# Kernel tuning notes

Hardware: AMD Instinct MI355X
Metric: run time of the kernel (lower is better)

The kernel has to match this reference:

```python
import jax, jax.numpy as jnp
import numpy as np

N = 100_000      # nodes
E = 1_600_000    # edges (avg degree 16)
D_IN = 64
D_HID = 64
D_OUT = 16


def setup_inputs() -> dict:
    key = jax.random.key(0)
    ks = jax.random.split(key, 12)
    x = jax.random.normal(ks[0], (N, D_IN), jnp.float32)
    edge_index = jax.random.randint(ks[1], (2, E), 0, N, dtype=jnp.int32)

    def lin(k, fan_in, fan_out):
        s = 1.0 / np.sqrt(fan_in)
        kw, kb = jax.random.split(k)
        W = jax.random.uniform(kw, (fan_in, fan_out), jnp.float32, -s, s)
        b = jax.random.uniform(kb, (fan_out,), jnp.float32, -s, s)
        return W, b

    W1, b1 = lin(ks[2], D_IN, D_HID)
    W2, b2 = lin(ks[3], D_HID, D_HID)
    W3, b3 = lin(ks[4], D_HID, D_HID)
    Wf1, bf1 = lin(ks[5], D_HID, D_HID)
    Wf2, bf2 = lin(ks[6], D_HID, D_OUT)
    return {"x": x, "edge_index": edge_index,
            "W1": W1, "b1": b1, "W2": W2, "b2": b2, "W3": W3, "b3": b3,
            "Wf1": Wf1, "bf1": bf1, "Wf2": Wf2, "bf2": bf2}


def _gcn_conv(x, src, dst, W, b):
    # PyG GCNConv: linear transform, add self-loops, symmetric deg^-1/2 norm,
    # scatter-add aggregation to targets, then bias.
    h = x @ W                                            # [N, d_out]
    ones = jnp.ones(src.shape[0], h.dtype)
    deg = jax.ops.segment_sum(ones, dst, num_segments=N) + 1.0  # +1 self-loop
    dinv = jax.lax.rsqrt(deg)                            # [N]
    coef = dinv[src] * dinv[dst]                         # [E]
    agg = jax.ops.segment_sum(h[src] * coef[:, None], dst, num_segments=N)
    agg = agg + h * (dinv * dinv)[:, None]               # self-loop messages
    return agg + b


def reference(x, edge_index, W1, b1, W2, b2, W3, b3, Wf1, bf1, Wf2, bf2):
    src, dst = edge_index[0], edge_index[1]
    # 3 stacked GCNConv layers; dropout p=0 -> identity
    h = jax.nn.relu(_gcn_conv(x, src, dst, W1, b1))
    h = jax.nn.relu(_gcn_conv(h, src, dst, W2, b2))
    h = jax.nn.relu(_gcn_conv(h, src, dst, W3, b3))
    # ffn: Linear -> ReLU -> Dropout(eval, identity) -> Linear
    h = jax.nn.relu(h @ Wf1 + bf1)
    pred = h @ Wf2 + bf2
    return pred
```

## Files before the change

### kernel.cpp

```cpp
#include <hip/hip_runtime.h>

#define NN   100000
#define EE   1600000
#define DD   64
#define DOUT 16
#define CAP  64
#define NPW  8
#define WPAD 68

#define BSH  9
#define NB   196
#define BCAP 10240
#define EPB  2048
#define NBL  ((EE + EPB - 1) / EPB)

__device__ __forceinline__ float lo16(unsigned u) {
    union { unsigned i; float f; } v; v.i = u << 16; return v.f;
}
__device__ __forceinline__ float hi16(unsigned u) {
    union { unsigned i; float f; } v; v.i = u & 0xffff0000u; return v.f;
}
__device__ __forceinline__ float bf2f(unsigned short h) {
    union { unsigned i; float f; } v; v.i = (unsigned)h << 16; return v.f;
}
__device__ __forceinline__ unsigned short f2bf(float f) {
    union { float f; unsigned i; } v; v.f = f;
    return (unsigned short)((v.i + 0x7fffu + ((v.i >> 16) & 1u)) >> 16);
}

__global__ __launch_bounds__(256) void k_scatter2(const int* __restrict__ ei,
                                                  int* __restrict__ gcur,
                                                  int2* __restrict__ bed,
                                                  unsigned* __restrict__ As,
                                                  unsigned* __restrict__ Bs) {
    if (blockIdx.x == 0) {
        int t = threadIdx.x;
        if (t < 32) As[(size_t)NN * 32 + t] = 0u;
        else if (t < 64) Bs[(size_t)NN * 32 + (t - 32)] = 0u;
    }
    __shared__ int h[NB];
    __shared__ int cur[NB];
    for (int i = threadIdx.x; i < NB; i += 256) h[i] = 0;
    __syncthreads();
    int e0 = blockIdx.x * EPB;
    int e1 = min(e0 + EPB, EE);
    for (int e = e0 + (int)threadIdx.x; e < e1; e += 256)
        atomicAdd(&h[ei[EE + e] >> BSH], 1);
    __syncthreads();
    for (int i = threadIdx.x; i < NB; i += 256)
        cur[i] = i * BCAP + (h[i] ? atomicAdd(&gcur[i], h[i]) : 0);
    __syncthreads();
    for (int e = e0 + (int)threadIdx.x; e < e1; e += 256) {
        int s = ei[e], d = ei[EE + e];
        int b = d >> BSH;
        int p = atomicAdd(&cur[b], 1);
        if (p < (b + 1) * BCAP) bed[p] = make_int2(s, d);
    }
}

__global__ __launch_bounds__(1024) void k_csr(const int2* __restrict__ bed,
                                              const int* __restrict__ gcur,
                                              const float* __restrict__ x,
                                              int* __restrict__ cnt,
                                              int* __restrict__ csr,
                                              unsigned* __restrict__ ts0) {
    __shared__ int lcnt[512];
    int b     = blockIdx.x;
    int nbase = b << BSH;
    int nmax  = min(512, NN - nbase);
    for (int i = threadIdx.x; i < 512; i += 1024) lcnt[i] = 0;
    __syncthreads();
    int lo = b * BCAP;
    int hi = lo + min(gcur[b], BCAP);
    for (int e = lo + (int)threadIdx.x; e < hi; e += 1024) {
        int2 sd = bed[e];
        int pos = atomicAdd(&lcnt[sd.y - nbase], 1);
        if (pos < CAP - 1) csr[(size_t)sd.y * CAP + pos + 1] = sd.x;
    }
    __syncthreads();
    for (int i = threadIdx.x; i < nmax; i += 1024) {
        int n = nbase + i;
        int c = lcnt[i];
        cnt[n] = c;
        if (c > 63) c = 63;
        int used = 1 + c;
        int end  = (used <= 32) ? 32 : 64;
        int* row = csr + (size_t)n * CAP;
        row[0] = n;
        for (int s = used; s < end; ++s) row[s] = NN;
    }
    const float2* xv = (const float2*)x;
    for (int idx = threadIdx.x; idx < nmax * 32; idx += 1024) {
        float dv = rsqrtf((float)lcnt[idx >> 5] + 1.0f);
        float2 v = xv[(size_t)nbase * 32 + idx];
        ts0[(size_t)nbase * 32 + idx] =
            (unsigned)f2bf(v.x * dv) | ((unsigned)f2bf(v.y * dv) << 16);
    }
}

__device__ __forceinline__ float4 gather_node(const uint2* __restrict__ hpv,
                                              const int* __restrict__ crow,
                                              int c, int sub, int m) {
    float4 fa = {0.f, 0.f, 0.f, 0.f}, fb = fa;
#define GROW(g, acc)                                                        \
    {                                                                       \
        int row = crow[4 * (g) + sub];                                      \
        uint2 U = hpv[((unsigned)row << 4) + m];                            \
        acc.x += lo16(U.x); acc.y += hi16(U.x);                             \
        acc.z += lo16(U.y); acc.w += hi16(U.y);                             \
    }
    GROW(0, fa) GROW(1, fb) GROW(2, fa) GROW(3, fb)
    GROW(4, fa) GROW(5, fb) GROW(6, fa) GROW(7, fb)
    if (c >= 32) {
#define GROW2(g, acc)                                                       \
        {                                                                   \
            int row = crow[32 + 4 * (g) + sub];                             \
            uint2 U = hpv[((unsigned)row << 4) + m];                        \
            acc.x += lo16(U.x); acc.y += hi16(U.x);                         \
            acc.z += lo16(U.y); acc.w += hi16(U.y);                         \
        }
        GROW2(0, fa) GROW2(1, fb) GROW2(2, fa) GROW2(3, fb)
        GROW2(4, fa) GROW2(5, fb) GROW2(6, fa) GROW2(7, fb)
#undef GROW2
    }
#undef GROW
    float4 s;
    s.x = fa.x + fb.x; s.y = fa.y + fb.y; s.z = fa.z + fb.z; s.w = fa.w + fb.w;
    s.x += __shfl_xor(s.x, 16); s.y += __shfl_xor(s.y, 16);
    s.z += __shfl_xor(s.z, 16); s.w += __shfl_xor(s.w, 16);
    s.x += __shfl_xor(s.x, 32); s.y += __shfl_xor(s.y, 32);
    s.z += __shfl_xor(s.z, 32); s.w += __shfl_xor(s.w, 32);
    return s;
}

__device__ __forceinline__ void stage_wt(const float* __restrict__ W,
                                         float* __restrict__ sWt, int tid) {
    for (int i = tid; i < DD * DD; i += 256) {
        int k = i >> 6, j = i & 63;
        sWt[j * WPAD + k] = W[i];
    }
}

template <int SCALE>
__global__ __launch_bounds__(256, 4) void k_layer(const unsigned short* __restrict__ tsin,
                                                  const int* __restrict__ csr,
                                                  const int* __restrict__ cnt,
                                                  const float* __restrict__ bias,
                                                  const float* __restrict__ W,
                                                  unsigned short* __restrict__ outp) {
    __shared__ float sWt[DD * WPAD];
    __shared__ float abuf[4][DD];
    const int lane = threadIdx.x & 63;
    const int wv   = threadIdx.x >> 6;
    const int sub  = lane >> 4;
    const int m    = lane & 15;

    stage_wt(W, sWt, threadIdx.x);
    __syncthreads();

    const float bv = bias[lane];
    const uint2* hpv   = (const uint2*)tsin;
    const float4* wcol = (const float4*)(sWt + lane * WPAD);

    int base = (blockIdx.x * 4 + wv) * NPW;
    for (int r = 0; r < NPW; ++r) {
        int n = base + r;
        if (n >= NN) return;
        int c = cnt[n]; if (c > 63) c = 63;
        float dv = rsqrtf((float)cnt[n] + 1.0f);
        float4 s = gather_node(hpv, csr + (size_t)n * CAP, c, sub, m);
        if (sub == 0) ((float4*)abuf[wv])[m] = s;

        const float4* ab = (const float4*)abuf[wv];
        float o = 0.f;
#pragma unroll
        for (int kk = 0; kk < DD / 4; ++kk) {
            float4 w = wcol[kk];
            float4 q = ab[kk];
            o = fmaf(q.x, w.x, fmaf(q.y, w.y, fmaf(q.z, w.z, fmaf(q.w, w.w, o))));
        }
        float t = fmaxf(fmaf(dv, o, bv), 0.f);
        outp[(size_t)n * DD + lane] = f2bf(SCALE ? t * dv : t);
    }
}

__global__ __launch_bounds__(256, 2) void k_ffn(const unsigned short* __restrict__ t3,
                                                const float* __restrict__ Wf1,
                                                const float* __restrict__ bf1,
                                                const float* __restrict__ Wf2,
                                                const float* __restrict__ bf2,
                                                float* __restrict__ out) {
    __shared__ float sW1t[DD * WPAD];
    __shared__ float tb8[4][NPW][DD];
    const int lane = threadIdx.x & 63;
    const int wv   = threadIdx.x >> 6;
    const int sub  = lane >> 4;
    const int m    = lane & 15;

    stage_wt(Wf1, sW1t, threadIdx.x);
    __syncthreads();

    float W2reg[16];
#pragma unroll
    for (int kk = 0; kk < 16; ++kk) W2reg[kk] = Wf2[(sub * 16 + kk) * DOUT + m];
    const float b1v = bf1[lane];
    const float b2v = bf2[m];
    const float4* w1col = (const float4*)(sW1t + lane * WPAD);

    int base = (blockIdx.x * 4 + wv) * NPW;

#pragma unroll
    for (int r = 0; r < NPW; ++r)
        tb8[wv][r][lane] = bf2f(t3[(size_t)(base + r) * DD + lane]);

    float u[NPW];
#pragma unroll
    for (int r = 0; r < NPW; ++r) u[r] = b1v;
#pragma unroll
    for (int kk = 0; kk < DD / 4; ++kk) {
        float4 w = w1col[kk];
#pragma unroll
        for (int r = 0; r < NPW; ++r) {
            float4 q = ((const float4*)tb8[wv][r])[kk];
            u[r] = fmaf(q.x, w.x, fmaf(q.y, w.y,
                    fmaf(q.z, w.z, fmaf(q.w, w.w, u[r]))));
        }
    }
#pragma unroll
    for (int r = 0; r < NPW; ++r)
        tb8[wv][r][lane] = fmaxf(u[r], 0.f);

    float p[NPW];
#pragma unroll
    for (int r = 0; r < NPW; ++r) p[r] = 0.f;
#pragma unroll
    for (int kq = 0; kq < 4; ++kq) {
        float a0 = W2reg[4 * kq + 0], a1 = W2reg[4 * kq + 1];
        float a2 = W2reg[4 * kq + 2], a3 = W2reg[4 * kq + 3];
#pragma unroll
        for (int r = 0; r < NPW; ++r) {
            float4 z = ((const float4*)(tb8[wv][r] + sub * 16))[kq];
            p[r] = fmaf(z.x, a0, fmaf(z.y, a1, fmaf(z.z, a2, fmaf(z.w, a3, p[r]))));
        }
    }
#pragma unroll
    for (int r = 0; r < NPW; ++r) {
        p[r] += __shfl_xor(p[r], 16);
        p[r] += __shfl_xor(p[r], 32);
        if (lane < 16) out[(size_t)(base + r) * DOUT + m] = p[r] + b2v;
    }
}

extern "C" void kernel_launch(void* const* d_in, const int* in_sizes, int n_in,
                              void* d_out, int out_size, void* d_ws, size_t ws_size,
                              hipStream_t stream) {
    const float* x   = (const float*)d_in[0];
    const int*   ei  = (const int*)d_in[1];
    const float* W1  = (const float*)d_in[2];
    const float* b1  = (const float*)d_in[3];
    const float* W2  = (const float*)d_in[4];
    const float* b2  = (const float*)d_in[5];
    const float* W3  = (const float*)d_in[6];
    const float* b3  = (const float*)d_in[7];
    const float* Wf1 = (const float*)d_in[8];
    const float* bf1 = (const float*)d_in[9];
    const float* Wf2 = (const float*)d_in[10];
    const float* bf2 = (const float*)d_in[11];
    float* out = (float*)d_out;

    char* ws = (char*)d_ws;
    auto al = [](size_t v) { return (v + 255) & ~(size_t)255; };
    size_t off = 0;
    int* cnt  = (int*)(ws + off);              off = al(off + (size_t)NN * 4);
    int* gcur = (int*)(ws + off);              off = al(off + (size_t)NB * 4);
    int* csr  = (int*)(ws + off);              off = al(off + (size_t)NN * CAP * 4);
    unsigned short* A = (unsigned short*)(ws + off); off = al(off + (size_t)(NN + 1) * DD * 2);
    unsigned short* B = (unsigned short*)(ws + off); off = al(off + (size_t)(NN + 1) * DD * 2);
    int2* bed = (int2*)(ws + off);             off = al(off + (size_t)NB * BCAP * 8);

    hipMemsetAsync(gcur, 0, (size_t)NB * 4, stream);
    k_scatter2<<<NBL, 256, 0, stream>>>(ei, gcur, bed, (unsigned*)A, (unsigned*)B);
    k_csr<<<NB, 1024, 0, stream>>>(bed, gcur, x, cnt, csr, (unsigned*)A);

    int gf = NN / (4 * NPW);

    k_layer<1><<<gf, 256, 0, stream>>>(A, csr, cnt, b1, W1, B);
    k_layer<1><<<gf, 256, 0, stream>>>(B, csr, cnt, b2, W2, A);
    k_layer<0><<<gf, 256, 0, stream>>>(A, csr, cnt, b3, W3, B);
    k_ffn<<<gf, 256, 0, stream>>>(B, Wf1, bf1, Wf2, bf2, out);
}
```

Baseline: 323.4 us.

## Pack bucketed edges into 32-bit words and use finer CSR buckets

Bucket width is halved to 256 nodes (391 buckets), and each bucketed edge is stored as one 32-bit word holding the source shifted left plus the destination offset within the bucket, replacing an int2. This halves the traffic of the intermediate edge buffer. The CSR build kernel uses 512-thread blocks over twice as many blocks, and the per-row padding fill is spread across threads instead of a serial per-node loop. The packing assumes source indices fit in 24 bits and bucket capacity still covers skewed degrees.

```diff
diff --git a/kernel.cpp b/kernel.cpp
--- a/kernel.cpp
+++ b/kernel.cpp
@@ -8,9 +8,9 @@
 #define NPW  8
 #define WPAD 68
 
-#define BSH  9
-#define NB   196
-#define BCAP 10240
+#define BSH  8
+#define NB   391
+#define BCAP 5120
 #define EPB  2048
 #define NBL  ((EE + EPB - 1) / EPB)
 
@@ -30,7 +30,7 @@
 
 __global__ __launch_bounds__(256) void k_scatter2(const int* __restrict__ ei,
                                                   int* __restrict__ gcur,
-                                                  int2* __restrict__ bed,
+                                                  unsigned* __restrict__ bed,
                                                   unsigned* __restrict__ As,
                                                   unsigned* __restrict__ Bs) {
     if (blockIdx.x == 0) {
@@ -54,43 +54,48 @@
         int s = ei[e], d = ei[EE + e];
         int b = d >> BSH;
         int p = atomicAdd(&cur[b], 1);
-        if (p < (b + 1) * BCAP) bed[p] = make_int2(s, d);
-    }
-}
-
-__global__ __launch_bounds__(1024) void k_csr(const int2* __restrict__ bed,
-                                              const int* __restrict__ gcur,
-                                              const float* __restrict__ x,
-                                              int* __restrict__ cnt,
-                                              int* __restrict__ csr,
-                                              unsigned* __restrict__ ts0) {
-    __shared__ int lcnt[512];
+        if (p < (b + 1) * BCAP)
+            bed[p] = ((unsigned)s << BSH) | (unsigned)(d & (255));
+    }
+}
+
+__global__ __launch_bounds__(512) void k_csr(const unsigned* __restrict__ bed,
+                                             const int* __restrict__ gcur,
+                                             const float* __restrict__ x,
+                                             int* __restrict__ cnt,
+                                             int* __restrict__ csr,
+                                             unsigned* __restrict__ ts0) {
+    __shared__ int lcnt[256];
     int b     = blockIdx.x;
     int nbase = b << BSH;
-    int nmax  = min(512, NN - nbase);
-    for (int i = threadIdx.x; i < 512; i += 1024) lcnt[i] = 0;
+    int nmax  = min(256, NN - nbase);
+    for (int i = threadIdx.x; i < 256; i += 512) lcnt[i] = 0;
     __syncthreads();
     int lo = b * BCAP;
     int hi = lo + min(gcur[b], BCAP);
-    for (int e = lo + (int)threadIdx.x; e < hi; e += 1024) {
-        int2 sd = bed[e];
-        int pos = atomicAdd(&lcnt[sd.y - nbase], 1);
-        if (pos < CAP - 1) csr[(size_t)sd.y * CAP + pos + 1] = sd.x;
-    }
-    __syncthreads();
-    for (int i = threadIdx.x; i < nmax; i += 1024) {
-        int n = nbase + i;
-        int c = lcnt[i];
-        cnt[n] = c;
-        if (c > 63) c = 63;
+    for (int e = lo + (int)threadIdx.x; e < hi; e += 512) {
+        unsigned v = bed[e];
+        int s    = (int)(v >> BSH);
+        int doff = (int)(v & 255);
+        int pos = atomicAdd(&lcnt[doff], 1);
+        if (pos < CAP - 1)
+            csr[(size_t)(nbase + doff) * CAP + pos + 1] = s;
+    }
+    __syncthreads();
+    for (int i = threadIdx.x; i < nmax; i += 512)
+        cnt[nbase + i] = lcnt[i];
+    for (int idx = threadIdx.x; idx < nmax * CAP; idx += 512) {
+        int i = idx >> 6, s = idx & 63;
+        int c = lcnt[i]; if (c > 63) c = 63;
         int used = 1 + c;
         int end  = (used <= 32) ? 32 : 64;
-        int* row = csr + (size_t)n * CAP;
-        row[0] = n;
-        for (int s = used; s < end; ++s) row[s] = NN;
+        if (s == 0)
+            csr[(size_t)(nbase + i) * CAP] = nbase + i;
+        else if (s >= used && s < end)
+            csr[(size_t)(nbase + i) * CAP + s] = NN;
     }
     const float2* xv = (const float2*)x;
-    for (int idx = threadIdx.x; idx < nmax * 32; idx += 1024) {
+    for (int idx = threadIdx.x; idx < nmax * 32; idx += 512) {
         float dv = rsqrtf((float)lcnt[idx >> 5] + 1.0f);
         float2 v = xv[(size_t)nbase * 32 + idx];
         ts0[(size_t)nbase * 32 + idx] =
@@ -276,11 +281,11 @@
     int* csr  = (int*)(ws + off);              off = al(off + (size_t)NN * CAP * 4);
     unsigned short* A = (unsigned short*)(ws + off); off = al(off + (size_t)(NN + 1) * DD * 2);
     unsigned short* B = (unsigned short*)(ws + off); off = al(off + (size_t)(NN + 1) * DD * 2);
-    int2* bed = (int2*)(ws + off);             off = al(off + (size_t)NB * BCAP * 8);
+    unsigned* bed = (unsigned*)(ws + off);     off = al(off + (size_t)NB * BCAP * 4);
 
     hipMemsetAsync(gcur, 0, (size_t)NB * 4, stream);
     k_scatter2<<<NBL, 256, 0, stream>>>(ei, gcur, bed, (unsigned*)A, (unsigned*)B);
-    k_csr<<<NB, 1024, 0, stream>>>(bed, gcur, x, cnt, csr, (unsigned*)A);
+    k_csr<<<NB, 512, 0, stream>>>(bed, gcur, x, cnt, csr, (unsigned*)A);
 
     int gf = NN / (4 * NPW);
 
```

Result: no change. 321.4 us (-0.6%).
